# Performance work log

Measured on AMD Instinct MI355X. Metric: run time of the kernel, lower is better.

## Reference

```python
import jax, jax.numpy as jnp
import numpy as np

TAU = 1.0

def setup_inputs() -> dict:
    key = jax.random.key(0)
    scores = jax.random.normal(key, (16, 2048), dtype=jnp.float32)
    return {"scores": scores}

def reference(scores):
    # scores: [B, n]
    B, n = scores.shape
    # row-sum of pairwise abs differences: Asum[b,i] = sum_k |s_i - s_k|
    Asum = jnp.sum(jnp.abs(scores[:, :, None] - scores[:, None, :]), axis=-1)  # [B, n]
    # scaling[j] = n + 1 - 2*(j+1)
    scaling = (n + 1 - 2 * (jnp.arange(n, dtype=jnp.float32) + 1.0))  # [n]
    # P_max[b, j, i] = s[b,i] * scaling[j] - Asum[b,i]
    P_max = scores[:, None, :] * scaling[None, :, None] - Asum[:, None, :]  # [B, n, n]
    P_hat = jax.nn.softmax(P_max / TAU, axis=-1)
    return P_hat
```

## Files before the change

### kernel.cpp

```cpp
#include <hip/hip_runtime.h>
#include <hip/hip_bf16.h>

#define N 2048
#define B 16
#define LOG2E 1.44269504088896340736f

typedef float v4f __attribute__((ext_vector_type(4)));

__global__ __launch_bounds__(256) void asum_kernel(const float* __restrict__ s,
                                                   float* __restrict__ asum2) {
    const int b = blockIdx.y;
    const int chunk = blockIdx.x;

    __shared__ float row[N];
    __shared__ float partial[256];
    const v4f* g4 = (const v4f*)(s + b * N);
    v4f* r4 = (v4f*)row;
    r4[threadIdx.x] = g4[threadIdx.x];
    r4[threadIdx.x + 256] = g4[threadIdx.x + 256];
    __syncthreads();

    const int il = threadIdx.x & 127;
    const int half = threadIdx.x >> 7;
    const int i = chunk * 128 + il;
    const float si = row[i];
    const v4f* row4 = (const v4f*)(row + half * (N / 2));
    float acc = 0.0f;
#pragma unroll 4
    for (int k = 0; k < N / 8; ++k) {
        v4f rv = row4[k];
        acc += fabsf(si - rv.x) + fabsf(si - rv.y) +
               fabsf(si - rv.z) + fabsf(si - rv.w);
    }
    partial[threadIdx.x] = acc;
    __syncthreads();
    if (threadIdx.x < 128)
        asum2[b * N + i] = LOG2E * (partial[threadIdx.x] + partial[threadIdx.x + 128]);
}

__global__ __launch_bounds__(256) void softmax_rows(const float* __restrict__ s,
                                                    const float* __restrict__ asum2,
                                                    float* __restrict__ out) {
    __shared__ float ls[N];
    __shared__ float la[N];

    const int t = threadIdx.x;
    const int lane = t & 63;
    const int wave = t >> 6;
    const int b = blockIdx.y;

    {
        const v4f* g4 = (const v4f*)(s + (size_t)b * N);
        const v4f* ga4 = (const v4f*)(asum2 + (size_t)b * N);
        v4f* l4 = (v4f*)ls;
        v4f* m4 = (v4f*)la;
        v4f s0 = g4[t], s1 = g4[t + 256];
        v4f a0 = ga4[t], a1 = ga4[t + 256];
        s0 *= LOG2E; s1 *= LOG2E;
        l4[t] = s0; l4[t + 256] = s1;
        m4[t] = a0; m4[t + 256] = a1;
    }
    __syncthreads();

    const v4f* ls4 = (const v4f*)ls;
    const v4f* la4 = (const v4f*)la;
    const int base = blockIdx.x * 32;

#pragma unroll 1
    for (int g = 0; g < 4; ++g) {
        const int jA = base + g * 8 + wave;
        const int jB = jA + 4;
        const float cA = (float)(N - 1 - 2 * jA);
        const float cB = (float)(N - 1 - 2 * jB);

        float va[32], vb[32];
#pragma unroll
        for (int c = 0; c < 8; ++c) {
            v4f sv = ls4[c * 64 + lane];
            v4f av = la4[c * 64 + lane];
            va[c * 4 + 0] = sv.x * cA - av.x;  vb[c * 4 + 0] = sv.x * cB - av.x;
            va[c * 4 + 1] = sv.y * cA - av.y;  vb[c * 4 + 1] = sv.y * cB - av.y;
            va[c * 4 + 2] = sv.z * cA - av.z;  vb[c * 4 + 2] = sv.z * cB - av.z;
            va[c * 4 + 3] = sv.w * cA - av.w;  vb[c * 4 + 3] = sv.w * cB - av.w;
        }

        float mA = va[0], mB = vb[0];
#pragma unroll
        for (int i = 1; i < 32; ++i) { mA = fmaxf(mA, va[i]); mB = fmaxf(mB, vb[i]); }
#pragma unroll
        for (int off = 32; off >= 1; off >>= 1) {
            mA = fmaxf(mA, __shfl_xor(mA, off));
            mB = fmaxf(mB, __shfl_xor(mB, off));
        }

        float sA = 0.0f, sB = 0.0f;
#pragma unroll
        for (int i = 0; i < 32; ++i) {
            va[i] = __builtin_amdgcn_exp2f(va[i] - mA);  sA += va[i];
            vb[i] = __builtin_amdgcn_exp2f(vb[i] - mB);  sB += vb[i];
        }
#pragma unroll
        for (int off = 32; off >= 1; off >>= 1) {
            sA += __shfl_xor(sA, off);
            sB += __shfl_xor(sB, off);
        }

        const float rA = 1.0f / sA;
        const float rB = 1.0f / sB;

        v4f* oA = (v4f*)(out + ((size_t)b * N + jA) * N);
        v4f* oB = (v4f*)(out + ((size_t)b * N + jB) * N);
#pragma unroll
        for (int c = 0; c < 8; ++c) {
            v4f o;
            o.x = va[c * 4 + 0] * rA; o.y = va[c * 4 + 1] * rA;
            o.z = va[c * 4 + 2] * rA; o.w = va[c * 4 + 3] * rA;
            __builtin_nontemporal_store(o, &oA[c * 64 + lane]);
            v4f p;
            p.x = vb[c * 4 + 0] * rB; p.y = vb[c * 4 + 1] * rB;
            p.z = vb[c * 4 + 2] * rB; p.w = vb[c * 4 + 3] * rB;
            __builtin_nontemporal_store(p, &oB[c * 64 + lane]);
        }
    }
}

extern "C" void kernel_launch(void* const* d_in, const int* in_sizes, int n_in,
                              void* d_out, int out_size, void* d_ws, size_t ws_size,
                              hipStream_t stream) {
    const float* scores = (const float*)d_in[0];
    float* out = (float*)d_out;
    float* asum2 = (float*)d_ws;

    dim3 g1(N / 128, B);
    asum_kernel<<<g1, 256, 0, stream>>>(scores, asum2);

    dim3 g2(N / 32, B);
    softmax_rows<<<g2, 256, 0, stream>>>(scores, asum2, out);
}
```

Baseline: 273.4 us.

## Split softmax into row-statistics pass and separate streaming write kernel

Replaces the single softmax kernel with two: one computes each row's max and reciprocal sum into workspace, and a second recomputes the exponentials and streams the normalized output with plain coalesced stores. The aim is to decouple the reduction from the 256MB output write so the store kernel carries less register pressure and saturates bandwidth. In exchange, every exp2 is computed twice, there is one more launch, and the output stores are no longer nontemporal.

```diff
diff --git a/kernel.cpp b/kernel.cpp
--- a/kernel.cpp
+++ b/kernel.cpp
@@ -38,9 +38,10 @@
         asum2[b * N + i] = LOG2E * (partial[threadIdx.x] + partial[threadIdx.x + 128]);
 }
 
-__global__ __launch_bounds__(256) void softmax_rows(const float* __restrict__ s,
-                                                    const float* __restrict__ asum2,
-                                                    float* __restrict__ out) {
+__global__ __launch_bounds__(256) void rowstat_kernel(const float* __restrict__ s,
+                                                      const float* __restrict__ asum2,
+                                                      float* __restrict__ m2,
+                                                      float* __restrict__ r2) {
     __shared__ float ls[N];
     __shared__ float la[N];
 
@@ -96,8 +97,8 @@
         float sA = 0.0f, sB = 0.0f;
 #pragma unroll
         for (int i = 0; i < 32; ++i) {
-            va[i] = __builtin_amdgcn_exp2f(va[i] - mA);  sA += va[i];
-            vb[i] = __builtin_amdgcn_exp2f(vb[i] - mB);  sB += vb[i];
+            sA += __builtin_amdgcn_exp2f(va[i] - mA);
+            sB += __builtin_amdgcn_exp2f(vb[i] - mB);
         }
 #pragma unroll
         for (int off = 32; off >= 1; off >>= 1) {
@@ -105,22 +106,66 @@
             sB += __shfl_xor(sB, off);
         }
 
-        const float rA = 1.0f / sA;
-        const float rB = 1.0f / sB;
+        if (lane == 0) {
+            m2[(size_t)b * N + jA] = mA;
+            r2[(size_t)b * N + jA] = 1.0f / sA;
+            m2[(size_t)b * N + jB] = mB;
+            r2[(size_t)b * N + jB] = 1.0f / sB;
+        }
+    }
+}
 
-        v4f* oA = (v4f*)(out + ((size_t)b * N + jA) * N);
-        v4f* oB = (v4f*)(out + ((size_t)b * N + jB) * N);
+__global__ __launch_bounds__(256) void stream_kernel(const float* __restrict__ s,
+                                                     const float* __restrict__ asum2,
+                                                     const float* __restrict__ m2,
+                                                     const float* __restrict__ r2,
+                                                     float* __restrict__ out) {
+    const int t = threadIdx.x;
+    const int b = blockIdx.y;
+    const int jbase = blockIdx.x * 16;
+
+    const float* sb = s + (size_t)b * N;
+    const float* ab = asum2 + (size_t)b * N;
+    v4f s0 = *(const v4f*)(sb + 4 * t);
+    v4f s1 = *(const v4f*)(sb + 1024 + 4 * t);
+    v4f a0 = *(const v4f*)(ab + 4 * t);
+    v4f a1 = *(const v4f*)(ab + 1024 + 4 * t);
+    s0 *= LOG2E; s1 *= LOG2E;
+
+    const v4f* mp = (const v4f*)(m2 + (size_t)b * N + jbase);
+    const v4f* rp = (const v4f*)(r2 + (size_t)b * N + jbase);
+    float mv[16], rv[16];
 #pragma unroll
-        for (int c = 0; c < 8; ++c) {
-            v4f o;
-            o.x = va[c * 4 + 0] * rA; o.y = va[c * 4 + 1] * rA;
-            o.z = va[c * 4 + 2] * rA; o.w = va[c * 4 + 3] * rA;
-            __builtin_nontemporal_store(o, &oA[c * 64 + lane]);
-            v4f p;
-            p.x = vb[c * 4 + 0] * rB; p.y = vb[c * 4 + 1] * rB;
-            p.z = vb[c * 4 + 2] * rB; p.w = vb[c * 4 + 3] * rB;
-            __builtin_nontemporal_store(p, &oB[c * 64 + lane]);
-        }
+    for (int q = 0; q < 4; ++q) {
+        v4f tm = mp[q];
+        v4f tr = rp[q];
+        mv[q * 4 + 0] = tm.x; mv[q * 4 + 1] = tm.y;
+        mv[q * 4 + 2] = tm.z; mv[q * 4 + 3] = tm.w;
+        rv[q * 4 + 0] = tr.x; rv[q * 4 + 1] = tr.y;
+        rv[q * 4 + 2] = tr.z; rv[q * 4 + 3] = tr.w;
+    }
+
+    float* ob = out + ((size_t)b * N + jbase) * N;
+
+#pragma unroll
+    for (int rr = 0; rr < 16; ++rr) {
+        const float cj = (float)(N - 1 - 2 * (jbase + rr));
+        const float m = mv[rr];
+        const float r = rv[rr];
+        v4f x0 = s0 * cj - a0;
+        v4f x1 = s1 * cj - a1;
+        v4f e0, e1;
+        e0.x = __builtin_amdgcn_exp2f(x0.x - m) * r;
+        e0.y = __builtin_amdgcn_exp2f(x0.y - m) * r;
+        e0.z = __builtin_amdgcn_exp2f(x0.z - m) * r;
+        e0.w = __builtin_amdgcn_exp2f(x0.w - m) * r;
+        e1.x = __builtin_amdgcn_exp2f(x1.x - m) * r;
+        e1.y = __builtin_amdgcn_exp2f(x1.y - m) * r;
+        e1.z = __builtin_amdgcn_exp2f(x1.z - m) * r;
+        e1.w = __builtin_amdgcn_exp2f(x1.w - m) * r;
+        float* op = ob + (size_t)rr * N;
+        *(v4f*)(op + 4 * t) = e0;
+        *(v4f*)(op + 1024 + 4 * t) = e1;
     }
 }
 
@@ -130,10 +175,15 @@
     const float* scores = (const float*)d_in[0];
     float* out = (float*)d_out;
     float* asum2 = (float*)d_ws;
+    float* m2 = (float*)d_ws + (size_t)B * N;
+    float* r2 = (float*)d_ws + 2 * (size_t)B * N;
 
     dim3 g1(N / 128, B);
     asum_kernel<<<g1, 256, 0, stream>>>(scores, asum2);
 
     dim3 g2(N / 32, B);
-    softmax_rows<<<g2, 256, 0, stream>>>(scores, asum2, out);
+    rowstat_kernel<<<g2, 256, 0, stream>>>(scores, asum2, m2, r2);
+
+    dim3 g3(N / 16, B);
+    stream_kernel<<<g3, 256, 0, stream>>>(scores, asum2, m2, r2, out);
 }
```

Result: no change. 276.8 us (+1.2%).
